# Performance work log

Hardware: AMD Instinct MI355X
Metric: run time of the kernel (lower is better)

## Reference

```python
import jax, jax.numpy as jnp
import numpy as np

# SS2D (VMamba) dims
B, H, W, C = 2, 48, 48, 96
D_INNER, D_STATE, DT_RANK, K = 192, 32, 6, 4


def _silu(x):
    return x * jax.nn.sigmoid(x)


def setup_inputs() -> dict:
    key = jax.random.key(0)
    ks = jax.random.split(key, 8)
    inputs = jax.random.normal(ks[0], (B, H, W, C), jnp.float32)
    in_proj_w = jax.random.normal(ks[1], (2 * D_INNER, C), jnp.float32) * 0.02
    conv_w = jax.random.normal(ks[2], (D_INNER, 1, 3, 3), jnp.float32) * 0.1
    conv_b = jnp.zeros((D_INNER,), jnp.float32)
    x_proj_w = jax.random.normal(ks[3], (K, DT_RANK + 2 * D_STATE, D_INNER), jnp.float32) * 0.02
    dt_projs_w = jax.random.normal(ks[4], (K, D_INNER, DT_RANK), jnp.float32) * 0.1
    dt_projs_b = jax.random.uniform(ks[5], (K, D_INNER), jnp.float32, -4.0, -2.0)
    # S4D-real init: A_log[n] = log(n+1), tiled over K*d_inner
    A_logs = jnp.log(jnp.tile(jnp.arange(1, D_STATE + 1, dtype=jnp.float32), (K * D_INNER, 1)))
    Ds = jnp.ones((K * D_INNER,), jnp.float32)
    ln_w = jnp.ones((D_INNER,), jnp.float32)
    ln_b = jnp.zeros((D_INNER,), jnp.float32)
    out_proj_w = jax.random.normal(ks[6], (C, D_INNER), jnp.float32) * 0.02
    return dict(inputs=inputs, in_proj_w=in_proj_w, conv_w=conv_w, conv_b=conv_b,
                x_proj_w=x_proj_w, dt_projs_w=dt_projs_w, dt_projs_b=dt_projs_b,
                A_logs=A_logs, Ds=Ds, ln_w=ln_w, ln_b=ln_b, out_proj_w=out_proj_w)


def _selective_scan(us, deltas, A, Bs, Cs, Ds_kd):
    # us, deltas: (B,K,d,L); Bs, Cs: (B,K,N,L); A: (K,d,N); Ds_kd: (K,d)
    u_l = jnp.moveaxis(us, -1, 0)      # (L,B,K,d)
    d_l = jnp.moveaxis(deltas, -1, 0)  # (L,B,K,d)
    B_l = jnp.moveaxis(Bs, -1, 0)      # (L,B,K,N)
    C_l = jnp.moveaxis(Cs, -1, 0)      # (L,B,K,N)
    h0 = jnp.zeros(us.shape[:3] + (A.shape[-1],), us.dtype)  # (B,K,d,N)

    def step(h, inp):
        u, d, b, c = inp
        dA = jnp.exp(d[..., None] * A)                    # (B,K,d,N)
        h = h * dA + (d * u)[..., None] * b[:, :, None, :]
        y = jnp.einsum('bkdn,bkn->bkd', h, c)
        return h, y

    _, ys = jax.lax.scan(step, h0, (u_l, d_l, B_l, C_l))
    ys = jnp.moveaxis(ys, 0, -1)  # (B,K,d,L)
    return ys + Ds_kd[None, :, :, None] * us


def _ss2d(x, in_proj_w, conv_w, conv_b, x_proj_w, dt_projs_w, dt_projs_b,
          A_logs, Ds, ln_w, ln_b, out_proj_w):
    b, h, w, c = x.shape
    L = h * w
    xz = jnp.einsum('bhwc,ec->bhwe', x, in_proj_w)          # (B,H,W,2*d_inner)
    x_, z = jnp.split(xz, 2, axis=-1)
    # depthwise 3x3 conv (NCHW), SAME padding
    x_ = jnp.transpose(x_, (0, 3, 1, 2))                    # (B,d,H,W)
    x_ = jax.lax.conv_general_dilated(x_, conv_w, (1, 1), 'SAME',
                                      feature_group_count=D_INNER,
                                      dimension_numbers=('NCHW', 'OIHW', 'NCHW'))
    x_ = _silu(x_ + conv_b[None, :, None, None])
    # 4-direction scan inputs
    x_hw = x_.reshape(b, D_INNER, L)
    x_wh = jnp.transpose(x_, (0, 1, 3, 2)).reshape(b, D_INNER, L)
    xs = jnp.stack([x_hw, x_wh], axis=1)                    # (B,2,d,L)
    xs = jnp.concatenate([xs, jnp.flip(xs, axis=-1)], axis=1)  # (B,4,d,L)
    x_dbl = jnp.einsum('bkdl,kcd->bkcl', xs, x_proj_w)      # (B,4,dt_rank+2N,L)
    dts = x_dbl[:, :, :DT_RANK]
    Bs = x_dbl[:, :, DT_RANK:DT_RANK + D_STATE]
    Cs = x_dbl[:, :, DT_RANK + D_STATE:]
    dts = jnp.einsum('bkrl,kdr->bkdl', dts, dt_projs_w)
    deltas = jax.nn.softplus(dts + dt_projs_b[None, :, :, None])
    A = -jnp.exp(A_logs).reshape(K, D_INNER, D_STATE)
    Ds_kd = Ds.reshape(K, D_INNER)
    out_y = _selective_scan(xs, deltas, A, Bs, Cs, Ds_kd)   # (B,4,d,L)
    inv_y = jnp.flip(out_y[:, 2:4], axis=-1)                # (B,2,d,L)
    wh_y = jnp.transpose(out_y[:, 1].reshape(b, D_INNER, w, h), (0, 1, 3, 2)).reshape(b, D_INNER, L)
    invwh_y = jnp.transpose(inv_y[:, 1].reshape(b, D_INNER, w, h), (0, 1, 3, 2)).reshape(b, D_INNER, L)
    y = out_y[:, 0] + inv_y[:, 0] + wh_y + invwh_y          # (B,d,L)
    y = jnp.transpose(y, (0, 2, 1)).reshape(b, h, w, D_INNER)
    # LayerNorm over channel dim
    mu = jnp.mean(y, axis=-1, keepdims=True)
    var = jnp.var(y, axis=-1, keepdims=True)
    y = (y - mu) * jax.lax.rsqrt(var + 1e-5) * ln_w + ln_b
    y = y * _silu(z)
    return jnp.einsum('bhwd,cd->bhwc', y, out_proj_w)


def reference(inputs, in_proj_w, conv_w, conv_b, x_proj_w, dt_projs_w, dt_projs_b,
              A_logs, Ds, ln_w, ln_b, out_proj_w):
    attn = _ss2d(inputs, in_proj_w, conv_w, conv_b, x_proj_w, dt_projs_w,
                 dt_projs_b, A_logs, Ds, ln_w, ln_b, out_proj_w)
    return inputs + attn
```

## Files before the change

### kernel.cpp

```cpp
#include <hip/hip_runtime.h>
#include <math.h>

#define B_ 2
#define H_ 48
#define W_ 48
#define C_ 96
#define D_ 192
#define L_ 2304
#define K_ 4
#define NS 32
#define RK 6
#define CD 70

#define NC 16
#define CL (L_/NC)
#define NCH (B_*K_*D_)

#define BDL (B_*D_*L_)
#define OFF_Z      0
#define OFF_XPRE   (OFF_Z    + BDL)
#define OFF_XHW    (OFF_XPRE + BDL)
#define OFF_XWH    (OFF_XHW  + BDL)
#define OFF_DELTA  (OFF_XWH  + BDL)
#define OFF_BS     (OFF_DELTA+ B_*K_*D_*L_)
#define OFF_CS     (OFF_BS   + B_*K_*L_*NS)
#define OFF_YS     (OFF_CS   + B_*K_*L_*NS)
#define OFF_YF     (OFF_YS   + B_*K_*L_*D_)

#define OFF_H0     OFF_YF

__global__ __launch_bounds__(256) void k1_inproj(const float* __restrict__ x,
        const float* __restrict__ w, float* __restrict__ ws) {
    __shared__ __align__(16) float Xs[24*128];
    int blk = blockIdx.x;
    int b = blk / 288;
    int rem = blk % 288;
    int l0 = (rem >> 2) * 32;
    int es = rem & 3;
    int tid = threadIdx.x;
    const float4* xs4 = (const float4*)(x + (size_t)(b*L_ + l0)*C_);
    #pragma unroll
    for (int it = 0; it < 3; ++it) {
        int i4 = it*256 + tid;
        float4 v = xs4[i4];
        int idx4 = i4*4;
        int p = idx4 / 96, c = idx4 % 96;
        *(float4*)&Xs[(c>>2)*128 + p*4] = v;
    }
    __syncthreads();
    int l = tid & 31, eg = tid >> 5;
    int pos = l0 + l;
    float acc[12];
    #pragma unroll
    for (int i = 0; i < 12; ++i) acc[i] = 0.f;
    const float4* wp[12];
    #pragma unroll
    for (int i = 0; i < 12; ++i) {
        int e = es*96 + eg*12 + i;
        wp[i] = (const float4*)(w + (size_t)e*96);
    }
    for (int q = 0; q < 24; ++q) {
        float4 xr = *(const float4*)&Xs[q*128 + l*4];
        #pragma unroll
        for (int i = 0; i < 12; ++i) {
            float4 wv = wp[i][q];
            acc[i] += xr.x*wv.x + xr.y*wv.y + xr.z*wv.z + xr.w*wv.w;
        }
    }
    if (es < 2) {
        float* xpre = ws + OFF_XPRE;
        #pragma unroll
        for (int i = 0; i < 12; ++i) {
            int e = es*96 + eg*12 + i;
            xpre[(size_t)(b*D_ + e)*L_ + pos] = acc[i];
        }
    } else {
        float* zp = ws + OFF_Z + (size_t)(b*L_ + pos)*D_ + (es-2)*96 + eg*12;
        #pragma unroll
        for (int q = 0; q < 3; ++q)
            *(float4*)&zp[q*4] = make_float4(acc[q*4], acc[q*4+1], acc[q*4+2], acc[q*4+3]);
    }
}

__global__ __launch_bounds__(256) void k2_conv(const float* __restrict__ cw,
        const float* __restrict__ cb, float* __restrict__ ws) {
    __shared__ float img[26*48];
    __shared__ float res[24*49];
    int blk = blockIdx.x;
    int bd = blk >> 1;
    int half = blk & 1;
    int d = bd % D_;
    int hh0 = half * 24;
    int tid = threadIdx.x;
    const float* xp = ws + OFF_XPRE + (size_t)bd*L_;
    for (int it = 0; it < 5; ++it) {
        int idx = it*256 + tid;
        if (idx < 26*48) {
            int gr = hh0 - 1 + idx/48;
            img[idx] = (gr >= 0 && gr < H_) ? xp[gr*48 + idx%48] : 0.f;
        }
    }
    float wr[9];
    #pragma unroll
    for (int j = 0; j < 9; ++j) wr[j] = cw[d*9 + j];
    float bias = cb[d];
    __syncthreads();
    float* hw = ws + OFF_XHW + (size_t)bd*L_ + hh0*48;
    for (int it = 0; it < 5; ++it) {
        int idx = it*256 + tid;
        if (idx < 24*48) {
            int r = idx/48, w0 = idx%48;
            float acc = bias;
            #pragma unroll
            for (int kh = 0; kh < 3; ++kh) {
                #pragma unroll
                for (int kw = 0; kw < 3; ++kw) {
                    int iw = w0 + kw - 1;
                    if (iw >= 0 && iw < W_)
                        acc = fmaf(img[(r+kh)*48 + iw], wr[kh*3 + kw], acc);
                }
            }
            float v = acc / (1.f + __expf(-acc));
            hw[idx] = v;
            res[r*49 + w0] = v;
        }
    }
    __syncthreads();
    float* wh = ws + OFF_XWH + (size_t)bd*L_;
    for (int it = 0; it < 5; ++it) {
        int idx = it*256 + tid;
        if (idx < 24*48) {
            int w0 = idx/24, r = idx%24;
            wh[w0*48 + hh0 + r] = res[r*49 + w0];
        }
    }
}

__global__ __launch_bounds__(256) void k3_xproj(const float* __restrict__ xpw,
        const float* __restrict__ dtw, const float* __restrict__ dtb,
        float* __restrict__ ws) {
    __shared__ __align__(16) float Xs[48*64];
    __shared__ float xd[CD*17];
    int blk = blockIdx.x;
    int b = blk / 576;
    int rem = blk % 576;
    int k = rem / 144;
    int l0 = (rem % 144) * 16;
    int tid = threadIdx.x;
    const float* src = ws + ((k & 1) ? OFF_XWH : OFF_XHW);
    bool flip = (k >= 2);
    #pragma unroll
    for (int it = 0; it < 12; ++it) {
        int idx = it*256 + tid;
        int d = idx >> 4, l = idx & 15;
        int pos = flip ? (L_ - 1 - (l0 + l)) : (l0 + l);
        Xs[(d>>2)*64 + l*4 + (d&3)] = src[(size_t)(b*D_ + d)*L_ + pos];
    }
    __syncthreads();
    int l = tid & 15, cg = tid >> 4;
    {
        float acc[5] = {0.f, 0.f, 0.f, 0.f, 0.f};
        const float4* wp[5];
        #pragma unroll
        for (int i = 0; i < 5; ++i) {
            int c = cg + 16*i;
            if (c >= CD) c = 0;
            wp[i] = (const float4*)(xpw + ((size_t)k*CD + c)*D_);
        }
        for (int q = 0; q < 48; ++q) {
            float4 xr = *(const float4*)&Xs[q*64 + l*4];
            #pragma unroll
            for (int i = 0; i < 5; ++i) {
                float4 wv = wp[i][q];
                acc[i] += xr.x*wv.x + xr.y*wv.y + xr.z*wv.z + xr.w*wv.w;
            }
        }
        #pragma unroll
        for (int i = 0; i < 5; ++i) {
            int c = cg + 16*i;
            if (c < CD) xd[c*17 + l] = acc[i];
        }
    }
    __syncthreads();
    {
        float r[6];
        #pragma unroll
        for (int rr = 0; rr < 6; ++rr) r[rr] = xd[rr*17 + l];
        float* dout = ws + OFF_DELTA + (size_t)(b*K_ + k)*D_*L_;
        int dg = tid >> 4;
        for (int i = 0; i < 12; ++i) {
            int d = dg*12 + i;
            const float* wdt = dtw + ((size_t)k*D_ + d)*6;
            float acc = dtb[k*D_ + d];
            #pragma unroll
            for (int rr = 0; rr < 6; ++rr) acc = fmaf(r[rr], wdt[rr], acc);
            float sp = fmaxf(acc, 0.f) + log1pf(__expf(-fabsf(acc)));
            dout[(size_t)d*L_ + l0 + l] = sp;
        }
    }
    {
        float* Bsp = ws + OFF_BS + ((size_t)(b*K_ + k)*L_ + l0)*NS;
        float* Csp = ws + OFF_CS + ((size_t)(b*K_ + k)*L_ + l0)*NS;
        int n = tid & 31, lq = tid >> 5;
        #pragma unroll
        for (int j = 0; j < 2; ++j) {
            int ll = lq + 8*j;
            Bsp[(size_t)ll*NS + n] = xd[(RK + n)*17 + ll];
            Csp[(size_t)ll*NS + n] = xd[(RK + NS + n)*17 + ll];
        }
    }
}

__global__ __launch_bounds__(512) void k4a_local(const float* __restrict__ Alogs,
        float* __restrict__ ws) {
    __shared__ float Pl[2][NC][NS];
    __shared__ float Hl[2][NC][NS];
    int blk = blockIdx.x;
    int bk = blk / 96;
    int p = blk % 96;
    int b = bk >> 2, k = bk & 3;
    int c = threadIdx.x >> 5;
    int n = threadIdx.x & 31;
    int dA = 2*p;
    float aA = -__expf(Alogs[((size_t)k*D_ + dA)*NS + n]);
    float aB = -__expf(Alogs[((size_t)k*D_ + dA + 1)*NS + n]);
    const float* dpA = ws + OFF_DELTA + (size_t)(bk*D_ + dA)*L_ + c*CL;
    const float* dpB = dpA + L_;
    const float* uA = ws + ((k & 1) ? OFF_XWH : OFF_XHW) + (size_t)(b*D_ + dA)*L_;
    const float* uB = uA + L_;
    const float* Bsp = ws + OFF_BS + ((size_t)bk*L_ + c*CL)*NS;
    bool flip = (k >= 2);
    float hA = 0.f, hB = 0.f, PA = 1.f, PB = 1.f;
    #pragma unroll 4
    for (int l = 0; l < CL; ++l) {
        int gl = c*CL + l;
        int gu = flip ? (L_ - 1 - gl) : gl;
        float dlA = dpA[l], dlB = dpB[l];
        float uAv = uA[gu], uBv = uB[gu];
        float bn = Bsp[l*NS + n];
        float eA = __expf(dlA * aA);
        float eB = __expf(dlB * aB);
        hA = fmaf(hA, eA, dlA*uAv*bn);
        hB = fmaf(hB, eB, dlB*uBv*bn);
        PA *= eA;
        PB *= eB;
    }
    Pl[0][c][n] = PA; Pl[1][c][n] = PB;
    Hl[0][c][n] = hA; Hl[1][c][n] = hB;
    __syncthreads();
    if (threadIdx.x < 64) {
        int ch = threadIdx.x >> 5, nn = threadIdx.x & 31;
        float* H0p = ws + OFF_H0 + (size_t)(bk*D_ + dA + ch)*NC*NS + nn;
        float h = 0.f;
        #pragma unroll
        for (int cc = 0; cc < NC; ++cc) {
            H0p[cc*NS] = h;
            h = fmaf(h, Pl[ch][cc][nn], Hl[ch][cc][nn]);
        }
    }
}

__global__ __launch_bounds__(512) void k4c_scan(const float* __restrict__ Alogs,
        const float* __restrict__ Dsp, float* __restrict__ ws) {
    __shared__ float yld[CL*32];
    int blk = blockIdx.x;
    int dg = blk % 6;
    int c  = (blk / 6) % NC;
    int bk = blk / (6*NC);
    int b = bk >> 2, k = bk & 3;
    int sw = threadIdx.x >> 5;
    int n  = threadIdx.x & 31;
    int dA = dg*32 + sw;
    int dB = dA + 16;
    float aA = -__expf(Alogs[((size_t)k*D_ + dA)*NS + n]);
    float aB = -__expf(Alogs[((size_t)k*D_ + dB)*NS + n]);
    float dcA = Dsp[k*D_ + dA];
    float dcB = Dsp[k*D_ + dB];
    const float* dpA = ws + OFF_DELTA + (size_t)(bk*D_ + dA)*L_ + c*CL;
    const float* dpB = dpA + 16*L_;
    const float* uA = ws + ((k & 1) ? OFF_XWH : OFF_XHW) + (size_t)(b*D_ + dA)*L_;
    const float* uB = uA + 16*L_;
    const float* Bsp = ws + OFF_BS + ((size_t)bk*L_ + c*CL)*NS;
    const float* Csp = ws + OFF_CS + ((size_t)bk*L_ + c*CL)*NS;
    bool flip = (k >= 2);
    float hA = ws[OFF_H0 + (size_t)(bk*D_ + dA)*NC*NS + c*NS + n];
    float hB = ws[OFF_H0 + (size_t)(bk*D_ + dB)*NC*NS + c*NS + n];
    int g = n >> 3;
    int off = ((g & 1) << 1) | (g >> 1);
    for (int lb = 0; lb < CL; lb += 4) {
        float yA[4], yB[4], uuA[4], uuB[4];
        #pragma unroll
        for (int j = 0; j < 4; ++j) {
            int l = lb + j;
            int gl = c*CL + l;
            int gu = flip ? (L_ - 1 - gl) : gl;
            float dlA = dpA[l], dlB = dpB[l];
            float uAv = uA[gu], uBv = uB[gu];
            float bn = Bsp[l*NS + n];
            float cn = Csp[l*NS + n];
            hA = fmaf(hA, __expf(dlA*aA), dlA*uAv*bn);
            hB = fmaf(hB, __expf(dlB*aB), dlB*uBv*bn);
            yA[j] = hA * cn; yB[j] = hB * cn;
            uuA[j] = uAv;    uuB[j] = uBv;
        }
        #pragma unroll
        for (int j = 0; j < 4; ++j) {
            yA[j] += __shfl_xor(yA[j], 16);
            yB[j] += __shfl_xor(yB[j], 16);
        }
        float zA0 = (n & 16) ? yA[1] : yA[0];
        float zA1 = (n & 16) ? yA[3] : yA[2];
        float zB0 = (n & 16) ? yB[1] : yB[0];
        float zB1 = (n & 16) ? yB[3] : yB[2];
        zA0 += __shfl_xor(zA0, 8); zA1 += __shfl_xor(zA1, 8);
        zB0 += __shfl_xor(zB0, 8); zB1 += __shfl_xor(zB1, 8);
        float wA = (n & 8) ? zA1 : zA0;
        float wB = (n & 8) ? zB1 : zB0;
        wA += __shfl_xor(wA, 4); wA += __shfl_xor(wA, 2); wA += __shfl_xor(wA, 1);
        wB += __shfl_xor(wB, 4); wB += __shfl_xor(wB, 2); wB += __shfl_xor(wB, 1);
        float uaA = (n & 16) ? uuA[1] : uuA[0];
        float ubA = (n & 16) ? uuA[3] : uuA[2];
        float usA = (n & 8) ? ubA : uaA;
        float uaB = (n & 16) ? uuB[1] : uuB[0];
        float ubB = (n & 16) ? uuB[3] : uuB[2];
        float usB = (n & 8) ? ubB : uaB;
        if ((n & 7) == 0) {
            yld[(lb + off)*32 + sw]      = fmaf(dcA, usA, wA);
            yld[(lb + off)*32 + sw + 16] = fmaf(dcB, usB, wB);
        }
    }
    __syncthreads();
    float* ysp = ws + OFF_YS + ((size_t)bk*L_ + c*CL)*D_ + dg*32;
    #pragma unroll
    for (int it = 0; it < 9; ++it) {
        int idx = it*512 + threadIdx.x;
        int l = idx >> 5, dd = idx & 31;
        ysp[(size_t)l*D_ + dd] = yld[idx];
    }
}

__global__ __launch_bounds__(192) void k5_combine(const float* __restrict__ lnw,
        const float* __restrict__ lnb, float* __restrict__ ws) {
    int bp = blockIdx.x;
    int b = bp / L_, pos = bp % L_;
    int d = threadIdx.x;
    int hh = pos / W_, w0 = pos % W_;
    int poswh = w0*H_ + hh;
    const float* ys = ws + OFF_YS + (size_t)b*K_*L_*D_;
    float y = ys[(size_t)(0*L_ + pos)*D_ + d]
            + ys[(size_t)(2*L_ + (L_ - 1 - pos))*D_ + d]
            + ys[(size_t)(1*L_ + poswh)*D_ + d]
            + ys[(size_t)(3*L_ + (L_ - 1 - poswh))*D_ + d];
    float s = y, ss = y*y;
    #pragma unroll
    for (int m = 32; m >= 1; m >>= 1) {
        s  += __shfl_xor(s, m);
        ss += __shfl_xor(ss, m);
    }
    __shared__ float red[2][4];
    int wv = threadIdx.x >> 6;
    if ((threadIdx.x & 63) == 0) { red[0][wv] = s; red[1][wv] = ss; }
    __syncthreads();
    float su = red[0][0] + red[0][1] + red[0][2];
    float sq = red[1][0] + red[1][1] + red[1][2];
    float mu  = su * (1.f/192.f);
    float var = sq * (1.f/192.f) - mu*mu;
    float rs  = rsqrtf(var + 1e-5f);
    float yn = (y - mu)*rs*lnw[d] + lnb[d];
    float zv = ws[OFF_Z + (size_t)(b*L_ + pos)*D_ + d];
    float sz = zv / (1.f + __expf(-zv));
    ws[OFF_YF + (size_t)(b*L_ + pos)*D_ + d] = yn * sz;
}

__global__ __launch_bounds__(256) void k6_outproj(const float* __restrict__ w,
        const float* __restrict__ xin, float* __restrict__ out,
        const float* __restrict__ ws) {
    __shared__ __align__(16) float Ys[48*64];
    __shared__ float outT[16*49];
    int blk = blockIdx.x;
    int b = blk / 288;
    int rem = blk % 288;
    int l0 = (rem >> 1) * 16;
    int es = rem & 1;
    int tid = threadIdx.x;
    const float4* yf4 = (const float4*)(ws + OFF_YF + (size_t)(b*L_ + l0)*D_);
    #pragma unroll
    for (int it = 0; it < 3; ++it) {
        int i4 = it*256 + tid;
        float4 v = yf4[i4];
        int idx4 = i4*4;
        int p = idx4 / 192, dd = idx4 % 192;
        *(float4*)&Ys[(dd>>2)*64 + p*4] = v;
    }
    __syncthreads();
    int l = tid & 15, cg = tid >> 4;
    float acc[3] = {0.f, 0.f, 0.f};
    const float4* wp[3];
    #pragma unroll
    for (int i = 0; i < 3; ++i) {
        int c = es*48 + cg*3 + i;
        wp[i] = (const float4*)(w + (size_t)c*D_);
    }
    for (int q = 0; q < 48; ++q) {
        float4 xr = *(const float4*)&Ys[q*64 + l*4];
        #pragma unroll
        for (int i = 0; i < 3; ++i) {
            float4 wv = wp[i][q];
            acc[i] += xr.x*wv.x + xr.y*wv.y + xr.z*wv.z + xr.w*wv.w;
        }
    }
    #pragma unroll
    for (int i = 0; i < 3; ++i) outT[l*49 + cg*3 + i] = acc[i];
    __syncthreads();
    #pragma unroll
    for (int it = 0; it < 3; ++it) {
        int idx = it*256 + tid;
        int p = idx / 48, cc = idx % 48;
        size_t o = (size_t)(b*L_ + l0 + p)*C_ + es*48 + cc;
        out[o] = xin[o] + outT[p*49 + cc];
    }
}

extern "C" void kernel_launch(void* const* d_in, const int* in_sizes, int n_in,
                              void* d_out, int out_size, void* d_ws, size_t ws_size,
                              hipStream_t stream) {
    const float* x        = (const float*)d_in[0];
    const float* in_proj  = (const float*)d_in[1];
    const float* conv_w   = (const float*)d_in[2];
    const float* conv_b   = (const float*)d_in[3];
    const float* x_proj_w = (const float*)d_in[4];
    const float* dt_w     = (const float*)d_in[5];
    const float* dt_b     = (const float*)d_in[6];
    const float* A_logs   = (const float*)d_in[7];
    const float* Ds       = (const float*)d_in[8];
    const float* ln_w     = (const float*)d_in[9];
    const float* ln_b     = (const float*)d_in[10];
    const float* out_w    = (const float*)d_in[11];
    float* out = (float*)d_out;
    float* ws  = (float*)d_ws;

    k1_inproj <<<576,  256, 0, stream>>>(x, in_proj, ws);
    k2_conv   <<<768,  256, 0, stream>>>(conv_w, conv_b, ws);
    k3_xproj  <<<1152, 256, 0, stream>>>(x_proj_w, dt_w, dt_b, ws);
    k4a_local <<<768,  512, 0, stream>>>(A_logs, ws);
    k4c_scan  <<<768,  512, 0, stream>>>(A_logs, Ds, ws);
    k5_combine<<<B_*L_,192, 0, stream>>>(ln_w, ln_b, ws);
    k6_outproj<<<576,  256, 0, stream>>>(out_w, x, out, ws);
}
```

Measured before the change: 284.2 us.

## Fuse chunked scan passes with decoupled look-back carry propagation between blocks

Merges the local chunk-reduction kernel and the chunked scan kernel into one kernel. Each block computes its chunk's local state and decay product, then waits on a flag from the previous chunk's block, builds its carry and publishes it before running the output scan. Flags are cleared in the x-projection kernel. This removes one launch and the H0 round trip through global memory, but it serialises carry passing across chunks and depends on blocks being scheduled in chunk-major order to avoid deadlock. The shared staging buffer is also padded to 33 columns to reduce bank conflicts.

```diff
diff --git a/kernel.cpp b/kernel.cpp
--- a/kernel.cpp
+++ b/kernel.cpp
@@ -27,7 +27,8 @@
 #define OFF_YS     (OFF_CS   + B_*K_*L_*NS)
 #define OFF_YF     (OFF_YS   + B_*K_*L_*D_)
 
-#define OFF_H0     OFF_YF
+#define OFF_HB     OFF_YF
+#define OFF_FLAG   (OFF_YF + 786432)
 
 __global__ __launch_bounds__(256) void k1_inproj(const float* __restrict__ x,
         const float* __restrict__ w, float* __restrict__ ws) {
@@ -142,6 +143,8 @@
     __shared__ __align__(16) float Xs[48*64];
     __shared__ float xd[CD*17];
     int blk = blockIdx.x;
+    if (blk < 768 && threadIdx.x == 0)
+        ((int*)(ws + OFF_FLAG))[blk] = 0;
     int b = blk / 576;
     int rem = blk % 576;
     int k = rem / 144;
@@ -211,62 +214,13 @@
     }
 }
 
-__global__ __launch_bounds__(512) void k4a_local(const float* __restrict__ Alogs,
-        float* __restrict__ ws) {
-    __shared__ float Pl[2][NC][NS];
-    __shared__ float Hl[2][NC][NS];
+__global__ __launch_bounds__(512) void k4f_scan(const float* __restrict__ Alogs,
+        const float* __restrict__ Dsp, float* __restrict__ ws) {
+    __shared__ float yld[CL*33];
     int blk = blockIdx.x;
-    int bk = blk / 96;
-    int p = blk % 96;
-    int b = bk >> 2, k = bk & 3;
-    int c = threadIdx.x >> 5;
-    int n = threadIdx.x & 31;
-    int dA = 2*p;
-    float aA = -__expf(Alogs[((size_t)k*D_ + dA)*NS + n]);
-    float aB = -__expf(Alogs[((size_t)k*D_ + dA + 1)*NS + n]);
-    const float* dpA = ws + OFF_DELTA + (size_t)(bk*D_ + dA)*L_ + c*CL;
-    const float* dpB = dpA + L_;
-    const float* uA = ws + ((k & 1) ? OFF_XWH : OFF_XHW) + (size_t)(b*D_ + dA)*L_;
-    const float* uB = uA + L_;
-    const float* Bsp = ws + OFF_BS + ((size_t)bk*L_ + c*CL)*NS;
-    bool flip = (k >= 2);
-    float hA = 0.f, hB = 0.f, PA = 1.f, PB = 1.f;
-    #pragma unroll 4
-    for (int l = 0; l < CL; ++l) {
-        int gl = c*CL + l;
-        int gu = flip ? (L_ - 1 - gl) : gl;
-        float dlA = dpA[l], dlB = dpB[l];
-        float uAv = uA[gu], uBv = uB[gu];
-        float bn = Bsp[l*NS + n];
-        float eA = __expf(dlA * aA);
-        float eB = __expf(dlB * aB);
-        hA = fmaf(hA, eA, dlA*uAv*bn);
-        hB = fmaf(hB, eB, dlB*uBv*bn);
-        PA *= eA;
-        PB *= eB;
-    }
-    Pl[0][c][n] = PA; Pl[1][c][n] = PB;
-    Hl[0][c][n] = hA; Hl[1][c][n] = hB;
-    __syncthreads();
-    if (threadIdx.x < 64) {
-        int ch = threadIdx.x >> 5, nn = threadIdx.x & 31;
-        float* H0p = ws + OFF_H0 + (size_t)(bk*D_ + dA + ch)*NC*NS + nn;
-        float h = 0.f;
-        #pragma unroll
-        for (int cc = 0; cc < NC; ++cc) {
-            H0p[cc*NS] = h;
-            h = fmaf(h, Pl[ch][cc][nn], Hl[ch][cc][nn]);
-        }
-    }
-}
-
-__global__ __launch_bounds__(512) void k4c_scan(const float* __restrict__ Alogs,
-        const float* __restrict__ Dsp, float* __restrict__ ws) {
-    __shared__ float yld[CL*32];
-    int blk = blockIdx.x;
+    int c  = blk / 48;
+    int bk = (blk % 48) / 6;
     int dg = blk % 6;
-    int c  = (blk / 6) % NC;
-    int bk = blk / (6*NC);
     int b = bk >> 2, k = bk & 3;
     int sw = threadIdx.x >> 5;
     int n  = threadIdx.x & 31;
@@ -283,8 +237,53 @@
     const float* Bsp = ws + OFF_BS + ((size_t)bk*L_ + c*CL)*NS;
     const float* Csp = ws + OFF_CS + ((size_t)bk*L_ + c*CL)*NS;
     bool flip = (k >= 2);
-    float hA = ws[OFF_H0 + (size_t)(bk*D_ + dA)*NC*NS + c*NS + n];
-    float hB = ws[OFF_H0 + (size_t)(bk*D_ + dB)*NC*NS + c*NS + n];
+
+    float hA = 0.f, hB = 0.f, PA = 1.f, PB = 1.f;
+    #pragma unroll 4
+    for (int l = 0; l < CL; ++l) {
+        int gl = c*CL + l;
+        int gu = flip ? (L_ - 1 - gl) : gl;
+        float dlA = dpA[l], dlB = dpB[l];
+        float uAv = uA[gu], uBv = uB[gu];
+        float bn = Bsp[l*NS + n];
+        float eA = __expf(dlA * aA);
+        float eB = __expf(dlB * aB);
+        hA = fmaf(hA, eA, dlA*uAv*bn);
+        hB = fmaf(hB, eB, dlB*uBv*bn);
+        PA *= eA;
+        PB *= eB;
+    }
+
+    float* Hbuf = ws + OFF_HB;
+    int* flg = (int*)(ws + OFF_FLAG);
+    int cell = (bk*6 + dg)*NC + c;
+    float h0A = 0.f, h0B = 0.f;
+    if (c > 0) {
+        if (threadIdx.x == 0) {
+            while (__hip_atomic_load(&flg[cell-1], __ATOMIC_ACQUIRE,
+                                     __HIP_MEMORY_SCOPE_AGENT) == 0) {
+                __builtin_amdgcn_s_sleep(4);
+            }
+        }
+        __syncthreads();
+        h0A = __hip_atomic_load(&Hbuf[(size_t)(cell-1)*1024 + sw*32 + n],
+                                __ATOMIC_RELAXED, __HIP_MEMORY_SCOPE_AGENT);
+        h0B = __hip_atomic_load(&Hbuf[(size_t)(cell-1)*1024 + (sw+16)*32 + n],
+                                __ATOMIC_RELAXED, __HIP_MEMORY_SCOPE_AGENT);
+    }
+    if (c < NC-1) {
+        __hip_atomic_store(&Hbuf[(size_t)cell*1024 + sw*32 + n],
+                           fmaf(h0A, PA, hA), __ATOMIC_RELAXED, __HIP_MEMORY_SCOPE_AGENT);
+        __hip_atomic_store(&Hbuf[(size_t)cell*1024 + (sw+16)*32 + n],
+                           fmaf(h0B, PB, hB), __ATOMIC_RELAXED, __HIP_MEMORY_SCOPE_AGENT);
+        __threadfence();
+        __syncthreads();
+        if (threadIdx.x == 0)
+            __hip_atomic_store(&flg[cell], 1, __ATOMIC_RELEASE,
+                               __HIP_MEMORY_SCOPE_AGENT);
+    }
+
+    hA = h0A; hB = h0B;
     int g = n >> 3;
     int off = ((g & 1) << 1) | (g >> 1);
     for (int lb = 0; lb < CL; lb += 4) {
@@ -325,8 +324,8 @@
         float ubB = (n & 16) ? uuB[3] : uuB[2];
         float usB = (n & 8) ? ubB : uaB;
         if ((n & 7) == 0) {
-            yld[(lb + off)*32 + sw]      = fmaf(dcA, usA, wA);
-            yld[(lb + off)*32 + sw + 16] = fmaf(dcB, usB, wB);
+            yld[(lb + off)*33 + sw]      = fmaf(dcA, usA, wA);
+            yld[(lb + off)*33 + sw + 16] = fmaf(dcB, usB, wB);
         }
     }
     __syncthreads();
@@ -335,7 +334,7 @@
     for (int it = 0; it < 9; ++it) {
         int idx = it*512 + threadIdx.x;
         int l = idx >> 5, dd = idx & 31;
-        ysp[(size_t)l*D_ + dd] = yld[idx];
+        ysp[(size_t)l*D_ + dd] = yld[l*33 + dd];
     }
 }
 
@@ -442,8 +441,7 @@
     k1_inproj <<<576,  256, 0, stream>>>(x, in_proj, ws);
     k2_conv   <<<768,  256, 0, stream>>>(conv_w, conv_b, ws);
     k3_xproj  <<<1152, 256, 0, stream>>>(x_proj_w, dt_w, dt_b, ws);
-    k4a_local <<<768,  512, 0, stream>>>(A_logs, ws);
-    k4c_scan  <<<768,  512, 0, stream>>>(A_logs, Ds, ws);
+    k4f_scan  <<<768,  512, 0, stream>>>(A_logs, Ds, ws);
     k5_combine<<<B_*L_,192, 0, stream>>>(ln_w, ln_b, ws);
     k6_outproj<<<576,  256, 0, stream>>>(out_w, x, out, ws);
 }
```

Result: slower. 794.8 us (+179.7%).

## Split scan kernels to one channel per warp with vector loads and exp2

Applied to the files above, without the earlier changes.

Both scan kernels now give each warp one channel instead of two, which doubles the grid size (1536 blocks for the chunk-local pass and 1536 for the full scan). This aims to raise parallelism and cut per-thread serial work. Delta and u are loaded as float4, with reversed loads for the flipped directions, and exp is replaced by a hardware exp2 on A prescaled by log2e. The chunk decay product is computed as exp2(a*sum(delta)) rather than as a running product. The trade-off is fewer independent chains per thread for latency hiding, and a padded LDS staging buffer for the ys writeback.

```diff
diff --git a/kernel.cpp b/kernel.cpp
--- a/kernel.cpp
+++ b/kernel.cpp
@@ -15,6 +15,15 @@
 #define NC 16
 #define CL (L_/NC)
 #define NCH (B_*K_*D_)
+#define LOG2E 1.44269504088896f
+
+__device__ __forceinline__ float fexp2(float x) {
+#if __has_builtin(__builtin_amdgcn_exp2f)
+    return __builtin_amdgcn_exp2f(x);
+#else
+    return __expf(x * 0.69314718055994531f);
+#endif
+}
 
 #define BDL (B_*D_*L_)
 #define OFF_Z      0
@@ -213,129 +222,120 @@
 
 __global__ __launch_bounds__(512) void k4a_local(const float* __restrict__ Alogs,
         float* __restrict__ ws) {
-    __shared__ float Pl[2][NC][NS];
-    __shared__ float Hl[2][NC][NS];
-    int blk = blockIdx.x;
-    int bk = blk / 96;
-    int p = blk % 96;
+    __shared__ float Pl[NC][NS];
+    __shared__ float Hl[NC][NS];
+    int blk = blockIdx.x;
+    int d = blk % D_;
+    int bk = blk / D_;
     int b = bk >> 2, k = bk & 3;
     int c = threadIdx.x >> 5;
     int n = threadIdx.x & 31;
-    int dA = 2*p;
-    float aA = -__expf(Alogs[((size_t)k*D_ + dA)*NS + n]);
-    float aB = -__expf(Alogs[((size_t)k*D_ + dA + 1)*NS + n]);
-    const float* dpA = ws + OFF_DELTA + (size_t)(bk*D_ + dA)*L_ + c*CL;
-    const float* dpB = dpA + L_;
-    const float* uA = ws + ((k & 1) ? OFF_XWH : OFF_XHW) + (size_t)(b*D_ + dA)*L_;
-    const float* uB = uA + L_;
+    float a2 = -__expf(Alogs[((size_t)k*D_ + d)*NS + n]) * LOG2E;
+    const float* dptr = ws + OFF_DELTA + (size_t)(bk*D_ + d)*L_ + c*CL;
+    const float* ubase = ws + ((k & 1) ? OFF_XWH : OFF_XHW) + (size_t)(b*D_ + d)*L_;
     const float* Bsp = ws + OFF_BS + ((size_t)bk*L_ + c*CL)*NS;
     bool flip = (k >= 2);
-    float hA = 0.f, hB = 0.f, PA = 1.f, PB = 1.f;
-    #pragma unroll 4
-    for (int l = 0; l < CL; ++l) {
-        int gl = c*CL + l;
-        int gu = flip ? (L_ - 1 - gl) : gl;
-        float dlA = dpA[l], dlB = dpB[l];
-        float uAv = uA[gu], uBv = uB[gu];
-        float bn = Bsp[l*NS + n];
-        float eA = __expf(dlA * aA);
-        float eB = __expf(dlB * aB);
-        hA = fmaf(hA, eA, dlA*uAv*bn);
-        hB = fmaf(hB, eB, dlB*uBv*bn);
-        PA *= eA;
-        PB *= eB;
-    }
-    Pl[0][c][n] = PA; Pl[1][c][n] = PB;
-    Hl[0][c][n] = hA; Hl[1][c][n] = hB;
-    __syncthreads();
-    if (threadIdx.x < 64) {
-        int ch = threadIdx.x >> 5, nn = threadIdx.x & 31;
-        float* H0p = ws + OFF_H0 + (size_t)(bk*D_ + dA + ch)*NC*NS + nn;
-        float h = 0.f;
+    float h = 0.f, sd = 0.f;
+    for (int lb = 0; lb < CL; lb += 4) {
+        float4 d4 = *(const float4*)(dptr + lb);
+        float4 t4;
+        if (!flip) {
+            t4 = *(const float4*)(ubase + c*CL + lb);
+        } else {
+            float4 r = *(const float4*)(ubase + (L_ - 4) - (c*CL + lb));
+            t4 = make_float4(r.w, r.z, r.y, r.x);
+        }
+        float dl[4] = {d4.x, d4.y, d4.z, d4.w};
+        float uu[4] = {t4.x, t4.y, t4.z, t4.w};
+        #pragma unroll
+        for (int j = 0; j < 4; ++j) {
+            float bn = Bsp[(lb + j)*NS + n];
+            float e = fexp2(dl[j]*a2);
+            h = fmaf(h, e, dl[j]*uu[j]*bn);
+            sd += dl[j];
+        }
+    }
+    Pl[c][n] = fexp2(a2*sd);
+    Hl[c][n] = h;
+    __syncthreads();
+    if (threadIdx.x < NS) {
+        float hh = 0.f;
         #pragma unroll
         for (int cc = 0; cc < NC; ++cc) {
-            H0p[cc*NS] = h;
-            h = fmaf(h, Pl[ch][cc][nn], Hl[ch][cc][nn]);
-        }
-    }
+            float p  = Pl[cc][n];
+            float hf = Hl[cc][n];
+            Pl[cc][n] = hh;
+            hh = fmaf(hh, p, hf);
+        }
+    }
+    __syncthreads();
+    ws[OFF_H0 + (size_t)(bk*D_ + d)*NC*NS + threadIdx.x] = Pl[c][n];
 }
 
 __global__ __launch_bounds__(512) void k4c_scan(const float* __restrict__ Alogs,
         const float* __restrict__ Dsp, float* __restrict__ ws) {
-    __shared__ float yld[CL*32];
-    int blk = blockIdx.x;
-    int dg = blk % 6;
-    int c  = (blk / 6) % NC;
-    int bk = blk / (6*NC);
+    __shared__ float yld[CL*17];
+    int blk = blockIdx.x;
+    int dg = blk % 12;
+    int c  = (blk / 12) % NC;
+    int bk = blk / (12*NC);
     int b = bk >> 2, k = bk & 3;
     int sw = threadIdx.x >> 5;
     int n  = threadIdx.x & 31;
-    int dA = dg*32 + sw;
-    int dB = dA + 16;
-    float aA = -__expf(Alogs[((size_t)k*D_ + dA)*NS + n]);
-    float aB = -__expf(Alogs[((size_t)k*D_ + dB)*NS + n]);
-    float dcA = Dsp[k*D_ + dA];
-    float dcB = Dsp[k*D_ + dB];
-    const float* dpA = ws + OFF_DELTA + (size_t)(bk*D_ + dA)*L_ + c*CL;
-    const float* dpB = dpA + 16*L_;
-    const float* uA = ws + ((k & 1) ? OFF_XWH : OFF_XHW) + (size_t)(b*D_ + dA)*L_;
-    const float* uB = uA + 16*L_;
+    int d = dg*16 + sw;
+    float a2 = -__expf(Alogs[((size_t)k*D_ + d)*NS + n]) * LOG2E;
+    float dc = Dsp[k*D_ + d];
+    const float* dptr = ws + OFF_DELTA + (size_t)(bk*D_ + d)*L_ + c*CL;
+    const float* ubase = ws + ((k & 1) ? OFF_XWH : OFF_XHW) + (size_t)(b*D_ + d)*L_;
     const float* Bsp = ws + OFF_BS + ((size_t)bk*L_ + c*CL)*NS;
     const float* Csp = ws + OFF_CS + ((size_t)bk*L_ + c*CL)*NS;
     bool flip = (k >= 2);
-    float hA = ws[OFF_H0 + (size_t)(bk*D_ + dA)*NC*NS + c*NS + n];
-    float hB = ws[OFF_H0 + (size_t)(bk*D_ + dB)*NC*NS + c*NS + n];
+    float h = ws[OFF_H0 + (size_t)(bk*D_ + d)*NC*NS + c*NS + n];
     int g = n >> 3;
     int off = ((g & 1) << 1) | (g >> 1);
     for (int lb = 0; lb < CL; lb += 4) {
-        float yA[4], yB[4], uuA[4], uuB[4];
+        float4 d4 = *(const float4*)(dptr + lb);
+        float4 t4;
+        if (!flip) {
+            t4 = *(const float4*)(ubase + c*CL + lb);
+        } else {
+            float4 r = *(const float4*)(ubase + (L_ - 4) - (c*CL + lb));
+            t4 = make_float4(r.w, r.z, r.y, r.x);
+        }
+        float dl[4] = {d4.x, d4.y, d4.z, d4.w};
+        float uu[4] = {t4.x, t4.y, t4.z, t4.w};
+        float y[4];
         #pragma unroll
         for (int j = 0; j < 4; ++j) {
-            int l = lb + j;
-            int gl = c*CL + l;
-            int gu = flip ? (L_ - 1 - gl) : gl;
-            float dlA = dpA[l], dlB = dpB[l];
-            float uAv = uA[gu], uBv = uB[gu];
-            float bn = Bsp[l*NS + n];
-            float cn = Csp[l*NS + n];
-            hA = fmaf(hA, __expf(dlA*aA), dlA*uAv*bn);
-            hB = fmaf(hB, __expf(dlB*aB), dlB*uBv*bn);
-            yA[j] = hA * cn; yB[j] = hB * cn;
-            uuA[j] = uAv;    uuB[j] = uBv;
-        }
-        #pragma unroll
-        for (int j = 0; j < 4; ++j) {
-            yA[j] += __shfl_xor(yA[j], 16);
-            yB[j] += __shfl_xor(yB[j], 16);
-        }
-        float zA0 = (n & 16) ? yA[1] : yA[0];
-        float zA1 = (n & 16) ? yA[3] : yA[2];
-        float zB0 = (n & 16) ? yB[1] : yB[0];
-        float zB1 = (n & 16) ? yB[3] : yB[2];
-        zA0 += __shfl_xor(zA0, 8); zA1 += __shfl_xor(zA1, 8);
-        zB0 += __shfl_xor(zB0, 8); zB1 += __shfl_xor(zB1, 8);
-        float wA = (n & 8) ? zA1 : zA0;
-        float wB = (n & 8) ? zB1 : zB0;
-        wA += __shfl_xor(wA, 4); wA += __shfl_xor(wA, 2); wA += __shfl_xor(wA, 1);
-        wB += __shfl_xor(wB, 4); wB += __shfl_xor(wB, 2); wB += __shfl_xor(wB, 1);
-        float uaA = (n & 16) ? uuA[1] : uuA[0];
-        float ubA = (n & 16) ? uuA[3] : uuA[2];
-        float usA = (n & 8) ? ubA : uaA;
-        float uaB = (n & 16) ? uuB[1] : uuB[0];
-        float ubB = (n & 16) ? uuB[3] : uuB[2];
-        float usB = (n & 8) ? ubB : uaB;
-        if ((n & 7) == 0) {
-            yld[(lb + off)*32 + sw]      = fmaf(dcA, usA, wA);
-            yld[(lb + off)*32 + sw + 16] = fmaf(dcB, usB, wB);
-        }
-    }
-    __syncthreads();
-    float* ysp = ws + OFF_YS + ((size_t)bk*L_ + c*CL)*D_ + dg*32;
-    #pragma unroll
-    for (int it = 0; it < 9; ++it) {
+            float bn = Bsp[(lb + j)*NS + n];
+            float cn = Csp[(lb + j)*NS + n];
+            float e = fexp2(dl[j]*a2);
+            h = fmaf(h, e, dl[j]*uu[j]*bn);
+            y[j] = h * cn;
+        }
+        #pragma unroll
+        for (int j = 0; j < 4; ++j) y[j] += __shfl_xor(y[j], 16);
+        float z0 = (n & 16) ? y[1] : y[0];
+        float z1 = (n & 16) ? y[3] : y[2];
+        z0 += __shfl_xor(z0, 8);
+        z1 += __shfl_xor(z1, 8);
+        float wv = (n & 8) ? z1 : z0;
+        wv += __shfl_xor(wv, 4);
+        wv += __shfl_xor(wv, 2);
+        wv += __shfl_xor(wv, 1);
+        float ua = (n & 16) ? uu[1] : uu[0];
+        float ub = (n & 16) ? uu[3] : uu[2];
+        float us = (n & 8) ? ub : ua;
+        if ((n & 7) == 0) yld[(lb + off)*17 + sw] = fmaf(dc, us, wv);
+    }
+    __syncthreads();
+    float* ysp = ws + OFF_YS + ((size_t)bk*L_ + c*CL)*D_ + dg*16;
+    for (int it = 0; it < 5; ++it) {
         int idx = it*512 + threadIdx.x;
-        int l = idx >> 5, dd = idx & 31;
-        ysp[(size_t)l*D_ + dd] = yld[idx];
+        if (idx < CL*16) {
+            int l = idx >> 4, dd = idx & 15;
+            ysp[(size_t)l*D_ + dd] = yld[l*17 + dd];
+        }
     }
 }
 
@@ -442,8 +442,8 @@
     k1_inproj <<<576,  256, 0, stream>>>(x, in_proj, ws);
     k2_conv   <<<768,  256, 0, stream>>>(conv_w, conv_b, ws);
     k3_xproj  <<<1152, 256, 0, stream>>>(x_proj_w, dt_w, dt_b, ws);
-    k4a_local <<<768,  512, 0, stream>>>(A_logs, ws);
-    k4c_scan  <<<768,  512, 0, stream>>>(A_logs, Ds, ws);
+    k4a_local <<<NCH,  512, 0, stream>>>(A_logs, ws);
+    k4c_scan  <<<1536, 512, 0, stream>>>(A_logs, Ds, ws);
     k5_combine<<<B_*L_,192, 0, stream>>>(ln_w, ln_b, ws);
     k6_outproj<<<576,  256, 0, stream>>>(out_w, x, out, ws);
 }
```

Result: no change. 289.5 us (+1.9%).
